# Performance work log

Hardware: AMD Instinct MI355X
Metric: run time of the kernel (lower is better)

## Reference

```python
import jax, jax.numpy as jnp
import numpy as np

N_NODES = 100000
N_EDGES = 1250000
IN_CH = 128
OUT_CH = 64


def setup_inputs() -> dict:
    key = jax.random.key(0)
    k1, k2, k3, k4 = jax.random.split(key, 4)
    x = jax.random.normal(k1, (N_NODES, IN_CH), dtype=jnp.float32)
    edge_index = jax.random.randint(k2, (2, N_EDGES), 0, N_NODES, dtype=jnp.int64)
    edge_weight = jax.random.uniform(k3, (N_EDGES,), dtype=jnp.float32)
    # Xavier-uniform weight, zero bias (as in reset_parameters)
    limit = float(np.sqrt(6.0 / (IN_CH + OUT_CH)))
    W = jax.random.uniform(k4, (IN_CH, OUT_CH), dtype=jnp.float32, minval=-limit, maxval=limit)
    b = jnp.zeros((OUT_CH,), dtype=jnp.float32)
    return {"x": x, "edge_index": edge_index, "edge_weight": edge_weight, "W": W, "b": b}


def reference(x, edge_index, edge_weight, W, b):
    # Dense transform: [N, in] @ [in, out] -> [N, out]
    h = jnp.matmul(x, W)
    row, col = edge_index[0], edge_index[1]
    n = h.shape[0]
    # Weighted in-degree via scatter-add on destination (row)
    deg = jnp.zeros((n,), dtype=h.dtype).at[row].add(edge_weight)
    # deg^-0.5 with inf (deg==0) replaced by 0
    deg_inv_sqrt = jnp.where(deg == 0, jnp.zeros_like(deg), deg ** -0.5)
    norm = deg_inv_sqrt[row] * deg_inv_sqrt[col]  # [E]
    # Gather source features, normalize, scatter-add to destinations
    out = jnp.zeros_like(h).at[row].add(h[col] * norm[:, None])
    return out + b
```

## Files before the change

kernel.cpp:

```cpp
#include <hip/hip_runtime.h>

#define N_NODES 100000
#define N_EDGES 1250000
#define IN_CH 128
#define OUT_CH 64

#define NPB 128
#define ACCS2 33
#define NBINS 782
#define LSTRIDE 783
#define RECCAP 2048
#define NB1 256
#define B1T 512
#define CH1 ((N_EDGES + NB1 - 1) / NB1)
#define MAXU ((CH1 + B1T - 1) / B1T)
#define GEMM_BLOCKS ((N_NODES + 127) / 128)

#define QSCALE 8192.0f
#define QBIAS_F 8388608.0f
#define QBIAS_U 8388608u
#define INV_QSCALE 1.220703125e-4f
#define SCALE_DEG 33554432.0f
#define INV_SCALE_DEG 2.9802322387695312e-08f

typedef __attribute__((ext_vector_type(8))) short short8;
typedef __attribute__((ext_vector_type(4))) float f32x4;

__device__ inline unsigned int f2bf(float f) {
    unsigned int u = __float_as_uint(f);
    unsigned int r = ((u >> 16) & 1u) + 0x7FFFu;
    return (u + r) >> 16;
}
__device__ inline float bf_lo(unsigned int p) { return __uint_as_float(p << 16); }
__device__ inline float bf_hi(unsigned int p) { return __uint_as_float(p & 0xFFFF0000u); }

__device__ inline unsigned long long qpacks(unsigned int p, float sc) {
    unsigned int lo = (unsigned int)__float2int_rn(fmaf(bf_lo(p), sc, QBIAS_F));
    unsigned int hi = (unsigned int)__float2int_rn(fmaf(bf_hi(p), sc, QBIAS_F));
    return ((unsigned long long)hi << 32) | (unsigned long long)lo;
}

__global__ __launch_bounds__(256) void init_kernel(const float* __restrict__ W,
                                                   unsigned int* __restrict__ Wb) {
    int g = blockIdx.x * 256 + threadIdx.x;
    int c = g >> 8;
    int t4 = (g >> 6) & 3;
    int l = g & 63;
    int q = l >> 4, r15 = l & 15;
    unsigned int o[4];
#pragma unroll
    for (int jj = 0; jj < 4; ++jj) {
        float f0 = W[(c * 32 + q * 8 + 2 * jj)     * OUT_CH + t4 * 16 + r15];
        float f1 = W[(c * 32 + q * 8 + 2 * jj + 1) * OUT_CH + t4 * 16 + r15];
        o[jj] = f2bf(f0) | (f2bf(f1) << 16);
    }
    *(uint4*)(Wb + (size_t)g * 4) = make_uint4(o[0], o[1], o[2], o[3]);
}

__global__ __launch_bounds__(512) void fused_kernel(const float* __restrict__ x,
                                                    const unsigned int* __restrict__ Wb,
                                                    const int* __restrict__ ei,
                                                    const float* __restrict__ ew,
                                                    int* __restrict__ lscan2d,
                                                    int2* __restrict__ brec,
                                                    unsigned int* __restrict__ hs) {
    __shared__ int2 srec[CH1];
    __shared__ int shist[NBINS];
    __shared__ int sscan[NBINS + 2];
    __shared__ int ssum[256];
    const int tid = threadIdx.x;

    if (blockIdx.x < NB1) {
        for (int i = tid; i < NBINS; i += B1T) shist[i] = 0;
        __syncthreads();

        const int e0 = blockIdx.x * CH1;
        const int total = (e0 + CH1 < N_EDGES) ? CH1 : N_EDGES - e0;

        int rowv[MAXU], colv[MAXU];
        float wv[MAXU];
#pragma unroll
        for (int u = 0; u < MAXU; ++u) {
            int e = e0 + tid + u * B1T;
            bool ok = (tid + u * B1T) < total;
            rowv[u] = ok ? ei[e] : -1;
            colv[u] = ok ? ei[N_EDGES + e] : 0;
            wv[u]   = ok ? ew[e] : 0.0f;
            if (ok) atomicAdd(&shist[rowv[u] >> 7], 1);
        }
        __syncthreads();

        int a0 = 0, a1 = 0, a2 = 0, a3 = 0, part = 0;
        const int b0 = tid * 4;
        if (tid < 256) {
            a0 = (b0 + 0 < NBINS) ? shist[b0 + 0] : 0;
            a1 = (b0 + 1 < NBINS) ? shist[b0 + 1] : 0;
            a2 = (b0 + 2 < NBINS) ? shist[b0 + 2] : 0;
            a3 = (b0 + 3 < NBINS) ? shist[b0 + 3] : 0;
            part = a0 + a1 + a2 + a3;
            ssum[tid] = part;
        }
        __syncthreads();
#pragma unroll
        for (int d = 1; d < 256; d <<= 1) {
            int add = 0;
            if (tid >= d && tid < 256) add = ssum[tid - d];
            __syncthreads();
            if (tid < 256) ssum[tid] += add;
            __syncthreads();
        }
        if (tid < 256) {
            int base = ssum[tid] - part;
            if (b0 + 0 <= NBINS) sscan[b0 + 0] = base;
            if (b0 + 1 <= NBINS) sscan[b0 + 1] = base + a0;
            if (b0 + 2 <= NBINS) sscan[b0 + 2] = base + a0 + a1;
            if (b0 + 3 <= NBINS) sscan[b0 + 3] = base + a0 + a1 + a2;
        }
        __syncthreads();

        for (int i = tid; i < NBINS; i += B1T) shist[i] = 0;
        __syncthreads();

#pragma unroll
        for (int u = 0; u < MAXU; ++u) {
            if (rowv[u] >= 0) {
                int bb = rowv[u] >> 7;
                int rk = atomicAdd(&shist[bb], 1);
                srec[sscan[bb] + rk] = make_int2(((rowv[u] & 127) << 17) | colv[u],
                                                 __float_as_int(wv[u]));
            }
        }
        __syncthreads();

        for (int i = tid; i < total; i += B1T) brec[e0 + i] = srec[i];
        int* lrow = lscan2d + blockIdx.x * LSTRIDE;
        for (int i = tid; i <= NBINS; i += B1T) lrow[i] = sscan[i];
    } else {
        const int blk  = blockIdx.x - NB1;
        const int w    = tid >> 6;
        const int lane = tid & 63;
        const int q    = lane >> 4, r15 = lane & 15;
        const int node = blk * 128 + w * 16 + r15;
        const int nl   = (node < N_NODES) ? node : N_NODES - 1;
        const float* xrow = x + (size_t)nl * IN_CH;

        f32x4 acc[4];
#pragma unroll
        for (int t = 0; t < 4; ++t) acc[t] = (f32x4){0.f, 0.f, 0.f, 0.f};

#pragma unroll
        for (int c = 0; c < 4; ++c) {
            float4 xa = *(const float4*)(xrow + c * 32 + q * 8);
            float4 xb = *(const float4*)(xrow + c * 32 + q * 8 + 4);
            short8 bfrag;
            bfrag[0] = (short)f2bf(xa.x); bfrag[1] = (short)f2bf(xa.y);
            bfrag[2] = (short)f2bf(xa.z); bfrag[3] = (short)f2bf(xa.w);
            bfrag[4] = (short)f2bf(xb.x); bfrag[5] = (short)f2bf(xb.y);
            bfrag[6] = (short)f2bf(xb.z); bfrag[7] = (short)f2bf(xb.w);
#pragma unroll
            for (int t = 0; t < 4; ++t) {
                short8 afrag = *(const short8*)(Wb + (size_t)((c * 4 + t) * 64 + lane) * 4);
                acc[t] = __builtin_amdgcn_mfma_f32_16x16x32_bf16(afrag, bfrag, acc[t], 0, 0, 0);
            }
        }

        if (node < N_NODES) {
#pragma unroll
            for (int t = 0; t < 4; ++t) {
                unsigned int p0 = f2bf(acc[t][0]) | (f2bf(acc[t][1]) << 16);
                unsigned int p1 = f2bf(acc[t][2]) | (f2bf(acc[t][3]) << 16);
                *(uint2*)(hs + (size_t)node * 32 + t * 8 + q * 2) = make_uint2(p0, p1);
            }
        }
    }
}

__global__ __launch_bounds__(256) void bin2_kernel(const int* __restrict__ lscan2d,
                                                   const int2* __restrict__ brec,
                                                   float* __restrict__ dis_g) {
    __shared__ int deg[NPB];
    const int t = threadIdx.x;
    const int b = blockIdx.x;
    if (t < NPB) deg[t] = 0;
    __syncthreads();

    int st = lscan2d[t * LSTRIDE + b];
    int en = lscan2d[t * LSTRIDE + b + 1];
    const int2* seg = brec + (size_t)t * CH1;
    for (int j = st; j < en; ++j) {
        int2 rec = seg[j];
        atomicAdd(&deg[rec.x >> 17], __float2int_rn(__int_as_float(rec.y) * SCALE_DEG));
    }
    __syncthreads();

    int node = b * NPB + t;
    if (t < NPB && node < N_NODES) {
        float d = (float)deg[t] * INV_SCALE_DEG;
        dis_g[node] = (d == 0.0f) ? 0.0f : (1.0f / sqrtf(d));
    }
}

__global__ __launch_bounds__(512) void gather_kernel(const int* __restrict__ lscan2d,
                                                     const int2* __restrict__ brec,
                                                     const uint4* __restrict__ hs,
                                                     const float* __restrict__ dis,
                                                     const float* __restrict__ b,
                                                     float* __restrict__ out) {
    __shared__ unsigned long long acc[NPB * ACCS2];
    __shared__ int cnt[NPB];
    __shared__ int recs[RECCAP];
    __shared__ int segoff[256];
    __shared__ int mtot_s;
    const int tid = threadIdx.x;
    const int blk = blockIdx.x;
    for (int k = tid; k < NPB * ACCS2; k += 512) acc[k] = 0ull;
    if (tid < NPB) cnt[tid] = 0;

    int st = 0, len = 0;
    if (tid < 256) {
        st  = lscan2d[tid * LSTRIDE + blk];
        len = lscan2d[tid * LSTRIDE + blk + 1] - st;
        segoff[tid] = len;
    }
    __syncthreads();
#pragma unroll
    for (int d = 1; d < 256; d <<= 1) {
        int add = 0;
        if (tid >= d && tid < 256) add = segoff[tid - d];
        __syncthreads();
        if (tid < 256) segoff[tid] += add;
        __syncthreads();
    }
    if (tid == 255) mtot_s = segoff[255];
    __syncthreads();
    int m = mtot_s;
    if (m > RECCAP) m = RECCAP;

    if (tid < 256) {
        int off = segoff[tid] - len;
        const int2* seg = brec + (size_t)tid * CH1 + st;
        for (int i = 0; i < len; ++i) {
            int p = off + i;
            if (p < RECCAP) recs[p] = seg[i].x;
        }
    }
    __syncthreads();

    const int wid = tid >> 6, lane = tid & 63;
    const int sub = lane >> 3, l8 = lane & 7;

    for (int j0 = wid * 32; j0 < m; j0 += 256) {
        bool ok[4];
        int rec[4];
        uint4 p[4];
        float sc[4];
#pragma unroll
        for (int s = 0; s < 4; ++s) {
            int jj = j0 + 8 * s + sub;
            ok[s] = jj < m;
            rec[s] = ok[s] ? recs[jj] : 0;
        }
#pragma unroll
        for (int s = 0; s < 4; ++s) {
            p[s] = ok[s] ? hs[(size_t)(rec[s] & 0x1FFFF) * 8 + l8]
                         : make_uint4(0, 0, 0, 0);
            sc[s] = ok[s] ? QSCALE * dis[rec[s] & 0x1FFFF] : 0.0f;
        }
#pragma unroll
        for (int s = 0; s < 4; ++s) {
            if (ok[s]) {
                int ba = (rec[s] >> 17) * ACCS2 + 4 * l8;
                atomicAdd(&acc[ba + 0], qpacks(p[s].x, sc[s]));
                atomicAdd(&acc[ba + 1], qpacks(p[s].y, sc[s]));
                atomicAdd(&acc[ba + 2], qpacks(p[s].z, sc[s]));
                atomicAdd(&acc[ba + 3], qpacks(p[s].w, sc[s]));
                if (l8 == 0) atomicAdd(&cnt[rec[s] >> 17], 1);
            }
        }
    }
    __syncthreads();

    const unsigned int* acc32 = (const unsigned int*)acc;
    float bc = b[lane];
    int half = lane & 1, slot = lane >> 1;
#pragma unroll 4
    for (int r = 0; r < 16; ++r) {
        int nl = wid * 16 + r;
        int node = blk * NPB + nl;
        if (node < N_NODES) {
            unsigned int raw = acc32[(nl * ACCS2 + slot) * 2 + half];
            int qsum = (int)(raw - (unsigned int)cnt[nl] * QBIAS_U);
            float di = dis[node] * INV_QSCALE;
            out[(size_t)node * OUT_CH + lane] = (float)qsum * di + bc;
        }
    }
}

extern "C" void kernel_launch(void* const* d_in, const int* in_sizes, int n_in,
                              void* d_out, int out_size, void* d_ws, size_t ws_size,
                              hipStream_t stream) {
    const float* x  = (const float*)d_in[0];
    const int*   ei = (const int*)d_in[1];
    const float* ew = (const float*)d_in[2];
    const float* W  = (const float*)d_in[3];
    const float* b  = (const float*)d_in[4];
    float* out = (float*)d_out;

    unsigned int* hs = (unsigned int*)d_ws;
    unsigned int* Wb = hs + (size_t)N_NODES * 32;
    int* lscan2d = (int*)(Wb + 4096);
    float* dis   = (float*)(lscan2d + NB1 * LSTRIDE);
    int2* brec   = (int2*)(dis + N_NODES);
    (void)ws_size; (void)in_sizes; (void)n_in; (void)out_size;

    init_kernel<<<4, 256, 0, stream>>>(W, Wb);
    fused_kernel<<<NB1 + GEMM_BLOCKS, 512, 0, stream>>>(x, Wb, ei, ew,
                                                        lscan2d, brec, hs);
    bin2_kernel<<<NBINS, 256, 0, stream>>>(lscan2d, brec, dis);
    gather_kernel<<<NBINS, 512, 0, stream>>>(lscan2d, brec, (const uint4*)hs,
                                             dis, b, out);
}
```

Before: 178.0 us.

## Compact per-bin edge records in prep kernel and slim gather kernel

Raises the number of first-pass binning blocks and replaces the serial per-thread segment walk in the degree kernel with a parallel, binary-search-based flattening of bin records. That prep kernel also counts in-edges per node through a packed 64-bit atomic and writes a compact per-bin source list. The gather kernel therefore no longer rescans segments or keeps per-node counters. This removes the duplicated prefix scan and serial segment reads from the gather, at the cost of an extra global write and read of the compacted records.

```diff
diff --git a/kernel.cpp b/kernel.cpp
--- a/kernel.cpp
+++ b/kernel.cpp
@@ -10,8 +10,9 @@
 #define NBINS 782
 #define LSTRIDE 783
 #define RECCAP 2048
-#define NB1 256
+#define NB1 384
 #define B1T 512
+#define BPT 384
 #define CH1 ((N_EDGES + NB1 - 1) / NB1)
 #define MAXU ((CH1 + B1T - 1) / B1T)
 #define GEMM_BLOCKS ((N_NODES + 127) / 128)
@@ -175,76 +176,81 @@
     }
 }
 
-__global__ __launch_bounds__(256) void bin2_kernel(const int* __restrict__ lscan2d,
-                                                   const int2* __restrict__ brec,
-                                                   float* __restrict__ dis_g) {
-    __shared__ int deg[NPB];
+__global__ __launch_bounds__(BPT) void binprep_kernel(const int* __restrict__ lscan2d,
+                                                      const int2* __restrict__ brec,
+                                                      int* __restrict__ brec2,
+                                                      float* __restrict__ dis,
+                                                      int* __restrict__ qcnt,
+                                                      int* __restrict__ mtot) {
+    __shared__ int sst[NB1];
+    __shared__ int segoff[NB1];
+    __shared__ int recs[RECCAP];
+    __shared__ unsigned long long degcnt[NPB];
     const int t = threadIdx.x;
     const int b = blockIdx.x;
-    if (t < NPB) deg[t] = 0;
+
+    if (t < NPB) degcnt[t] = 0ull;
+    {
+        int st  = lscan2d[t * LSTRIDE + b];
+        int en  = lscan2d[t * LSTRIDE + b + 1];
+        sst[t] = st;
+        segoff[t] = en - st;
+    }
     __syncthreads();
-
-    int st = lscan2d[t * LSTRIDE + b];
-    int en = lscan2d[t * LSTRIDE + b + 1];
-    const int2* seg = brec + (size_t)t * CH1;
-    for (int j = st; j < en; ++j) {
-        int2 rec = seg[j];
-        atomicAdd(&deg[rec.x >> 17], __float2int_rn(__int_as_float(rec.y) * SCALE_DEG));
+#pragma unroll
+    for (int d = 1; d < NB1; d <<= 1) {
+        int add = (t >= d) ? segoff[t - d] : 0;
+        __syncthreads();
+        segoff[t] += add;
+        __syncthreads();
+    }
+    const int m = segoff[NB1 - 1];
+
+    for (int p = t; p < m; p += BPT) {
+        int lo = 0, hi = NB1 - 1;
+        while (lo < hi) {
+            int mid = (lo + hi) >> 1;
+            if (segoff[mid] > p) hi = mid; else lo = mid + 1;
+        }
+        int excl = (lo == 0) ? 0 : segoff[lo - 1];
+        int2 rec = brec[(size_t)lo * CH1 + sst[lo] + (p - excl)];
+        if (p < RECCAP) recs[p] = rec.x;
+        unsigned int qd = (unsigned int)__float2int_rn(__int_as_float(rec.y) * SCALE_DEG);
+        atomicAdd(&degcnt[rec.x >> 17],
+                  (1ull << 32) | (unsigned long long)qd);
     }
     __syncthreads();
 
-    int node = b * NPB + t;
-    if (t < NPB && node < N_NODES) {
-        float d = (float)deg[t] * INV_SCALE_DEG;
-        dis_g[node] = (d == 0.0f) ? 0.0f : (1.0f / sqrtf(d));
-    }
-}
-
-__global__ __launch_bounds__(512) void gather_kernel(const int* __restrict__ lscan2d,
-                                                     const int2* __restrict__ brec,
+    if (t < NPB) {
+        int node = b * NPB + t;
+        if (node < N_NODES) {
+            unsigned long long dc = degcnt[t];
+            float d = (float)(unsigned int)dc * INV_SCALE_DEG;
+            dis[node]  = (d == 0.0f) ? 0.0f : (1.0f / sqrtf(d));
+            qcnt[node] = (int)(dc >> 32);
+        }
+    }
+    int mc = (m < RECCAP) ? m : RECCAP;
+    if (t == 0) mtot[b] = mc;
+    for (int p = t; p < mc; p += BPT)
+        brec2[(size_t)b * RECCAP + p] = recs[p];
+}
+
+__global__ __launch_bounds__(512) void gather_kernel(const int* __restrict__ mtot,
+                                                     const int* __restrict__ brec2,
                                                      const uint4* __restrict__ hs,
                                                      const float* __restrict__ dis,
+                                                     const int* __restrict__ qcnt,
                                                      const float* __restrict__ b,
                                                      float* __restrict__ out) {
     __shared__ unsigned long long acc[NPB * ACCS2];
-    __shared__ int cnt[NPB];
-    __shared__ int recs[RECCAP];
-    __shared__ int segoff[256];
-    __shared__ int mtot_s;
     const int tid = threadIdx.x;
     const int blk = blockIdx.x;
     for (int k = tid; k < NPB * ACCS2; k += 512) acc[k] = 0ull;
-    if (tid < NPB) cnt[tid] = 0;
-
-    int st = 0, len = 0;
-    if (tid < 256) {
-        st  = lscan2d[tid * LSTRIDE + blk];
-        len = lscan2d[tid * LSTRIDE + blk + 1] - st;
-        segoff[tid] = len;
-    }
     __syncthreads();
-#pragma unroll
-    for (int d = 1; d < 256; d <<= 1) {
-        int add = 0;
-        if (tid >= d && tid < 256) add = segoff[tid - d];
-        __syncthreads();
-        if (tid < 256) segoff[tid] += add;
-        __syncthreads();
-    }
-    if (tid == 255) mtot_s = segoff[255];
-    __syncthreads();
-    int m = mtot_s;
-    if (m > RECCAP) m = RECCAP;
-
-    if (tid < 256) {
-        int off = segoff[tid] - len;
-        const int2* seg = brec + (size_t)tid * CH1 + st;
-        for (int i = 0; i < len; ++i) {
-            int p = off + i;
-            if (p < RECCAP) recs[p] = seg[i].x;
-        }
-    }
-    __syncthreads();
+
+    const int m = mtot[blk];
+    const int rbase = blk * RECCAP;
 
     const int wid = tid >> 6, lane = tid & 63;
     const int sub = lane >> 3, l8 = lane & 7;
@@ -258,7 +264,7 @@
         for (int s = 0; s < 4; ++s) {
             int jj = j0 + 8 * s + sub;
             ok[s] = jj < m;
-            rec[s] = ok[s] ? recs[jj] : 0;
+            rec[s] = ok[s] ? brec2[rbase + jj] : 0;
         }
 #pragma unroll
         for (int s = 0; s < 4; ++s) {
@@ -274,7 +280,6 @@
                 atomicAdd(&acc[ba + 1], qpacks(p[s].y, sc[s]));
                 atomicAdd(&acc[ba + 2], qpacks(p[s].z, sc[s]));
                 atomicAdd(&acc[ba + 3], qpacks(p[s].w, sc[s]));
-                if (l8 == 0) atomicAdd(&cnt[rec[s] >> 17], 1);
             }
         }
     }
@@ -289,7 +294,7 @@
         int node = blk * NPB + nl;
         if (node < N_NODES) {
             unsigned int raw = acc32[(nl * ACCS2 + slot) * 2 + half];
-            int qsum = (int)(raw - (unsigned int)cnt[nl] * QBIAS_U);
+            int qsum = (int)(raw - (unsigned int)qcnt[node] * QBIAS_U);
             float di = dis[node] * INV_QSCALE;
             out[(size_t)node * OUT_CH + lane] = (float)qsum * di + bc;
         }
@@ -309,14 +314,17 @@
     unsigned int* hs = (unsigned int*)d_ws;
     unsigned int* Wb = hs + (size_t)N_NODES * 32;
     int* lscan2d = (int*)(Wb + 4096);
-    float* dis   = (float*)(lscan2d + NB1 * LSTRIDE);
-    int2* brec   = (int2*)(dis + N_NODES);
+    int* mtot    = lscan2d + (size_t)NB1 * LSTRIDE;
+    float* dis   = (float*)(mtot + 800);
+    int* qcnt    = (int*)(dis + N_NODES);
+    int* brec2   = qcnt + N_NODES;
+    int2* brec   = (int2*)(brec2 + (size_t)NBINS * RECCAP);
     (void)ws_size; (void)in_sizes; (void)n_in; (void)out_size;
 
     init_kernel<<<4, 256, 0, stream>>>(W, Wb);
     fused_kernel<<<NB1 + GEMM_BLOCKS, 512, 0, stream>>>(x, Wb, ei, ew,
                                                         lscan2d, brec, hs);
-    bin2_kernel<<<NBINS, 256, 0, stream>>>(lscan2d, brec, dis);
-    gather_kernel<<<NBINS, 512, 0, stream>>>(lscan2d, brec, (const uint4*)hs,
-                                             dis, b, out);
-}
+    binprep_kernel<<<NBINS, BPT, 0, stream>>>(lscan2d, brec, brec2, dis, qcnt, mtot);
+    gather_kernel<<<NBINS, 512, 0, stream>>>(mtot, brec2, (const uint4*)hs,
+                                             dis, qcnt, b, out);
+}
```

Measured after the change: 159.7 us. -10.3%, faster.
